# Optimization experiments

Hardware: AMD Instinct MI355X
Metric: run time of the kernel (lower is better)

Reference implementation:

```python
import jax, jax.numpy as jnp
import numpy as np


def setup_inputs() -> dict:
    key = jax.random.key(0)
    k1, k2, k3, k4, k5 = jax.random.split(key, 5)
    N, E, D = 100000, 600000, 128
    h = jax.random.normal(k1, (N, D), dtype=jnp.float32)
    src = jax.random.randint(k2, (E,), 0, N, dtype=jnp.int64)
    dst = jax.random.randint(k3, (E,), 0, N, dtype=jnp.int64)
    W_w = jax.random.normal(k4, (D, D), dtype=jnp.float32) * (1.0 / np.sqrt(D))
    W_b = jax.random.normal(k5, (D,), dtype=jnp.float32) * 0.01
    return {"h": h, "src": src, "dst": dst, "W_w": W_w, "W_b": W_b}


def reference(h, src, dst, W_w, W_b):
    # Project all node features once (N x D GEMM), then gather per edge.
    # score_e = sum_d (W h[src_e] + b)_d * h[dst_e]_d
    Wh = h @ W_w.T + W_b            # [N, D]
    scores = jnp.sum(Wh[src] * h[dst], axis=-1)  # [E]
    return scores
```

## Files before the change

kernel.cpp:

```cpp
#include <hip/hip_runtime.h>
#include <hip/hip_bf16.h>

#define D 128

typedef __attribute__((ext_vector_type(8))) short bf16x8;
typedef __attribute__((ext_vector_type(4))) float f32x4;

__device__ __forceinline__ unsigned int f2bf_bits(float f) {
    union { float f; unsigned int u; } c; c.f = f;
    return (c.u + 0x7fffu + ((c.u >> 16) & 1u)) >> 16;
}
__device__ __forceinline__ unsigned int pack2bf(float a, float b) {
    return f2bf_bits(a) | (f2bf_bits(b) << 16);
}
__device__ __forceinline__ float bf_lo(unsigned int u) {
    union { unsigned int u; float f; } c; c.u = u << 16; return c.f;
}
__device__ __forceinline__ float bf_hi(unsigned int u) {
    union { unsigned int u; float f; } c; c.u = u & 0xffff0000u; return c.f;
}

__global__ __launch_bounds__(256) void wh_mfma_kernel(
    const float* __restrict__ h, const float* __restrict__ W,
    const float* __restrict__ bias, ushort* __restrict__ Wh_bf,
    ushort* __restrict__ h_bf, int N)
{
    __shared__ alignas(16) unsigned char lds_h[64 * 256];
    __shared__ alignas(16) unsigned char lds_w[128 * 256];

    const int t = threadIdx.x;
    const int nodeBase = blockIdx.x * 64;

#pragma unroll
    for (int it = 0; it < 8; ++it) {
        const int idx = t + 256 * it;
        const int row = idx >> 5;
        const int seg = idx & 31;
        const int node = nodeBase + row;
        float4 x = make_float4(0.f, 0.f, 0.f, 0.f);
        if (node < N)
            x = reinterpret_cast<const float4*>(h)[(size_t)node * 32 + seg];
        const uint2 p = make_uint2(pack2bf(x.x, x.y), pack2bf(x.z, x.w));
        const int boff = (seg * 8) ^ ((row & 7) << 4);
        *reinterpret_cast<uint2*>(&lds_h[row * 256 + boff]) = p;
        if (node < N)
            *reinterpret_cast<uint2*>(h_bf + (size_t)node * D + seg * 4) = p;
    }
#pragma unroll
    for (int it = 0; it < 16; ++it) {
        const int idx = t + 256 * it;
        const int row = idx >> 5;
        const int seg = idx & 31;
        const float4 x = reinterpret_cast<const float4*>(W)[idx];
        const uint2 p = make_uint2(pack2bf(x.x, x.y), pack2bf(x.z, x.w));
        const int boff = (seg * 8) ^ ((row & 7) << 4);
        *reinterpret_cast<uint2*>(&lds_w[row * 256 + boff]) = p;
    }
    __syncthreads();

    const int lane = t & 63;
    const int wv   = t >> 6;
    const int lr   = lane & 15;
    const int g    = lane >> 4;

    bf16x8 afrag[4];
    {
        const int row = wv * 16 + lr;
#pragma unroll
        for (int kt = 0; kt < 4; ++kt) {
            const int boff = (kt * 64 + g * 16) ^ ((row & 7) << 4);
            afrag[kt] = *reinterpret_cast<const bf16x8*>(&lds_h[row * 256 + boff]);
        }
    }

#pragma unroll
    for (int ct = 0; ct < 8; ++ct) {
        const int wrow = ct * 16 + lr;
        const float bb = bias[wrow];
        f32x4 acc = {bb, bb, bb, bb};
#pragma unroll
        for (int kt = 0; kt < 4; ++kt) {
            const int boff = (kt * 64 + g * 16) ^ ((wrow & 7) << 4);
            const bf16x8 bfrag =
                *reinterpret_cast<const bf16x8*>(&lds_w[wrow * 256 + boff]);
            acc = __builtin_amdgcn_mfma_f32_16x16x32_bf16(afrag[kt], bfrag, acc, 0, 0, 0);
        }
        const int node0 = nodeBase + wv * 16 + g * 4;
#pragma unroll
        for (int r = 0; r < 4; ++r) {
            if (node0 + r < N)
                Wh_bf[(size_t)(node0 + r) * D + wrow] = (ushort)f2bf_bits(acc[r]);
        }
    }
}

__global__ __launch_bounds__(256) void edge_score_kernel(
    const ushort* __restrict__ Wh_bf, const ushort* __restrict__ h_bf,
    const int* __restrict__ src, const int* __restrict__ dst,
    float* __restrict__ out, int E)
{
    const long long t = (long long)blockIdx.x * blockDim.x + threadIdx.x;
    const int e = (int)(t >> 4);
    const int l = (int)(t & 15);
    if (e >= E) return;

    const int s = src[e];
    const int d = dst[e];

    const uint4 av = reinterpret_cast<const uint4*>(Wh_bf + (size_t)s * D)[l];
    const uint4 bv = reinterpret_cast<const uint4*>(h_bf  + (size_t)d * D)[l];

    float acc = 0.f;
    acc = fmaf(bf_lo(av.x), bf_lo(bv.x), acc);
    acc = fmaf(bf_hi(av.x), bf_hi(bv.x), acc);
    acc = fmaf(bf_lo(av.y), bf_lo(bv.y), acc);
    acc = fmaf(bf_hi(av.y), bf_hi(bv.y), acc);
    acc = fmaf(bf_lo(av.z), bf_lo(bv.z), acc);
    acc = fmaf(bf_hi(av.z), bf_hi(bv.z), acc);
    acc = fmaf(bf_lo(av.w), bf_lo(bv.w), acc);
    acc = fmaf(bf_hi(av.w), bf_hi(bv.w), acc);

#pragma unroll
    for (int m = 8; m > 0; m >>= 1)
        acc += __shfl_xor(acc, m, 64);

    if (l == 0) out[e] = acc;
}

extern "C" void kernel_launch(void* const* d_in, const int* in_sizes, int n_in,
                              void* d_out, int out_size, void* d_ws, size_t ws_size,
                              hipStream_t stream)
{
    const float* h   = (const float*)d_in[0];
    const int*   src = (const int*)  d_in[1];
    const int*   dst = (const int*)  d_in[2];
    const float* W   = (const float*)d_in[3];
    const float* b   = (const float*)d_in[4];
    float* out = (float*)d_out;

    const int N = in_sizes[0] / D;
    const int E = in_sizes[1];

    ushort* Wh_bf = (ushort*)d_ws;
    ushort* h_bf  = (ushort*)d_ws + (size_t)N * D;

    {
        const int blocks = (N + 63) / 64;
        wh_mfma_kernel<<<blocks, 256, 0, stream>>>(h, W, b, Wh_bf, h_bf, N);
    }
    {
        const long long total = (long long)E * 16;
        const int blocks = (int)((total + 255) / 256);
        edge_score_kernel<<<blocks, 256, 0, stream>>>(Wh_bf, h_bf, src, dst, out, E);
    }
}
```

Baseline: 151.0 us.

## Persist GEMM blocks over node tiles and process two edges per 8-lane group

The projection kernel becomes persistent with a grid capped at 768 blocks. Each block converts W into LDS once and loops over 64-node tiles, so the per-block W load and bf16 conversion are amortised. The edge kernel now gives each 8-lane group two edges, with 32 bytes per lane per row, and writes both scores with a single float2 store. That cuts the shuffle reduction and raises memory-level parallelism per thread. bf16 packing switches to the HIP intrinsic conversion. The costs are an extra barrier per tile and less grid-level parallelism in the GEMM.

```diff
diff --git a/kernel.cpp b/kernel.cpp
--- a/kernel.cpp
+++ b/kernel.cpp
@@ -11,7 +11,9 @@
     return (c.u + 0x7fffu + ((c.u >> 16) & 1u)) >> 16;
 }
 __device__ __forceinline__ unsigned int pack2bf(float a, float b) {
-    return f2bf_bits(a) | (f2bf_bits(b) << 16);
+    union { __hip_bfloat162 h; unsigned int u; } c;
+    c.h = __float22bfloat162_rn(make_float2(a, b));
+    return c.u;
 }
 __device__ __forceinline__ float bf_lo(unsigned int u) {
     union { unsigned int u; float f; } c; c.u = u << 16; return c.f;
@@ -20,32 +22,28 @@
     union { unsigned int u; float f; } c; c.u = u & 0xffff0000u; return c.f;
 }
 
+__device__ __forceinline__ float dot8(uint4 a, uint4 b, float acc) {
+    acc = fmaf(bf_lo(a.x), bf_lo(b.x), acc);
+    acc = fmaf(bf_hi(a.x), bf_hi(b.x), acc);
+    acc = fmaf(bf_lo(a.y), bf_lo(b.y), acc);
+    acc = fmaf(bf_hi(a.y), bf_hi(b.y), acc);
+    acc = fmaf(bf_lo(a.z), bf_lo(b.z), acc);
+    acc = fmaf(bf_hi(a.z), bf_hi(b.z), acc);
+    acc = fmaf(bf_lo(a.w), bf_lo(b.w), acc);
+    acc = fmaf(bf_hi(a.w), bf_hi(b.w), acc);
+    return acc;
+}
+
 __global__ __launch_bounds__(256) void wh_mfma_kernel(
     const float* __restrict__ h, const float* __restrict__ W,
     const float* __restrict__ bias, ushort* __restrict__ Wh_bf,
-    ushort* __restrict__ h_bf, int N)
+    ushort* __restrict__ h_bf, int N, int numTiles)
 {
     __shared__ alignas(16) unsigned char lds_h[64 * 256];
     __shared__ alignas(16) unsigned char lds_w[128 * 256];
 
     const int t = threadIdx.x;
-    const int nodeBase = blockIdx.x * 64;
 
-#pragma unroll
-    for (int it = 0; it < 8; ++it) {
-        const int idx = t + 256 * it;
-        const int row = idx >> 5;
-        const int seg = idx & 31;
-        const int node = nodeBase + row;
-        float4 x = make_float4(0.f, 0.f, 0.f, 0.f);
-        if (node < N)
-            x = reinterpret_cast<const float4*>(h)[(size_t)node * 32 + seg];
-        const uint2 p = make_uint2(pack2bf(x.x, x.y), pack2bf(x.z, x.w));
-        const int boff = (seg * 8) ^ ((row & 7) << 4);
-        *reinterpret_cast<uint2*>(&lds_h[row * 256 + boff]) = p;
-        if (node < N)
-            *reinterpret_cast<uint2*>(h_bf + (size_t)node * D + seg * 4) = p;
-    }
 #pragma unroll
     for (int it = 0; it < 16; ++it) {
         const int idx = t + 256 * it;
@@ -56,41 +54,62 @@
         const int boff = (seg * 8) ^ ((row & 7) << 4);
         *reinterpret_cast<uint2*>(&lds_w[row * 256 + boff]) = p;
     }
-    __syncthreads();
 
     const int lane = t & 63;
     const int wv   = t >> 6;
     const int lr   = lane & 15;
     const int g    = lane >> 4;
 
-    bf16x8 afrag[4];
-    {
-        const int row = wv * 16 + lr;
-#pragma unroll
-        for (int kt = 0; kt < 4; ++kt) {
-            const int boff = (kt * 64 + g * 16) ^ ((row & 7) << 4);
-            afrag[kt] = *reinterpret_cast<const bf16x8*>(&lds_h[row * 256 + boff]);
-        }
-    }
+    for (int tile = blockIdx.x; tile < numTiles; tile += gridDim.x) {
+        const int nodeBase = tile * 64;
 
 #pragma unroll
-    for (int ct = 0; ct < 8; ++ct) {
-        const int wrow = ct * 16 + lr;
-        const float bb = bias[wrow];
-        f32x4 acc = {bb, bb, bb, bb};
+        for (int it = 0; it < 8; ++it) {
+            const int idx = t + 256 * it;
+            const int row = idx >> 5;
+            const int seg = idx & 31;
+            const int node = nodeBase + row;
+            float4 x = make_float4(0.f, 0.f, 0.f, 0.f);
+            if (node < N)
+                x = reinterpret_cast<const float4*>(h)[(size_t)node * 32 + seg];
+            const uint2 p = make_uint2(pack2bf(x.x, x.y), pack2bf(x.z, x.w));
+            const int boff = (seg * 8) ^ ((row & 7) << 4);
+            *reinterpret_cast<uint2*>(&lds_h[row * 256 + boff]) = p;
+            if (node < N)
+                *reinterpret_cast<uint2*>(h_bf + (size_t)node * D + seg * 4) = p;
+        }
+        __syncthreads();
+
+        bf16x8 afrag[4];
+        {
+            const int row = wv * 16 + lr;
 #pragma unroll
-        for (int kt = 0; kt < 4; ++kt) {
-            const int boff = (kt * 64 + g * 16) ^ ((wrow & 7) << 4);
-            const bf16x8 bfrag =
-                *reinterpret_cast<const bf16x8*>(&lds_w[wrow * 256 + boff]);
-            acc = __builtin_amdgcn_mfma_f32_16x16x32_bf16(afrag[kt], bfrag, acc, 0, 0, 0);
+            for (int kt = 0; kt < 4; ++kt) {
+                const int boff = (kt * 64 + g * 16) ^ ((row & 7) << 4);
+                afrag[kt] = *reinterpret_cast<const bf16x8*>(&lds_h[row * 256 + boff]);
+            }
         }
-        const int node0 = nodeBase + wv * 16 + g * 4;
+
 #pragma unroll
-        for (int r = 0; r < 4; ++r) {
-            if (node0 + r < N)
-                Wh_bf[(size_t)(node0 + r) * D + wrow] = (ushort)f2bf_bits(acc[r]);
+        for (int ct = 0; ct < 8; ++ct) {
+            const int wrow = ct * 16 + lr;
+            const float bb = bias[wrow];
+            f32x4 acc = {bb, bb, bb, bb};
+#pragma unroll
+            for (int kt = 0; kt < 4; ++kt) {
+                const int boff = (kt * 64 + g * 16) ^ ((wrow & 7) << 4);
+                const bf16x8 bfrag =
+                    *reinterpret_cast<const bf16x8*>(&lds_w[wrow * 256 + boff]);
+                acc = __builtin_amdgcn_mfma_f32_16x16x32_bf16(afrag[kt], bfrag, acc, 0, 0, 0);
+            }
+            const int node0 = nodeBase + wv * 16 + g * 4;
+#pragma unroll
+            for (int r = 0; r < 4; ++r) {
+                if (node0 + r < N)
+                    Wh_bf[(size_t)(node0 + r) * D + wrow] = (ushort)f2bf_bits(acc[r]);
+            }
         }
+        __syncthreads();
     }
 }
 
@@ -100,31 +119,48 @@
     float* __restrict__ out, int E)
 {
     const long long t = (long long)blockIdx.x * blockDim.x + threadIdx.x;
-    const int e = (int)(t >> 4);
-    const int l = (int)(t & 15);
-    if (e >= E) return;
+    const int grp = (int)(t >> 3);
+    const int l   = (int)(t & 7);
+    const int e0  = grp * 2;
+    if (e0 >= E) return;
+    const int e1 = e0 + 1;
+    const bool has1 = e1 < E;
 
-    const int s = src[e];
-    const int d = dst[e];
+    const int s0 = src[e0], d0 = dst[e0];
+    const int s1 = has1 ? src[e1] : s0;
+    const int d1 = has1 ? dst[e1] : d0;
 
-    const uint4 av = reinterpret_cast<const uint4*>(Wh_bf + (size_t)s * D)[l];
-    const uint4 bv = reinterpret_cast<const uint4*>(h_bf  + (size_t)d * D)[l];
+    const uint4* A0 = reinterpret_cast<const uint4*>(Wh_bf + (size_t)s0 * D);
+    const uint4* B0 = reinterpret_cast<const uint4*>(h_bf  + (size_t)d0 * D);
+    const uint4* A1 = reinterpret_cast<const uint4*>(Wh_bf + (size_t)s1 * D);
+    const uint4* B1 = reinterpret_cast<const uint4*>(h_bf  + (size_t)d1 * D);
 
-    float acc = 0.f;
-    acc = fmaf(bf_lo(av.x), bf_lo(bv.x), acc);
-    acc = fmaf(bf_hi(av.x), bf_hi(bv.x), acc);
-    acc = fmaf(bf_lo(av.y), bf_lo(bv.y), acc);
-    acc = fmaf(bf_hi(av.y), bf_hi(bv.y), acc);
-    acc = fmaf(bf_lo(av.z), bf_lo(bv.z), acc);
-    acc = fmaf(bf_hi(av.z), bf_hi(bv.z), acc);
-    acc = fmaf(bf_lo(av.w), bf_lo(bv.w), acc);
-    acc = fmaf(bf_hi(av.w), bf_hi(bv.w), acc);
+    const uint4 a0a = A0[2 * l];
+    const uint4 a0b = A0[2 * l + 1];
+    const uint4 b0a = B0[2 * l];
+    const uint4 b0b = B0[2 * l + 1];
+    const uint4 a1a = A1[2 * l];
+    const uint4 a1b = A1[2 * l + 1];
+    const uint4 b1a = B1[2 * l];
+    const uint4 b1b = B1[2 * l + 1];
+
+    float acc0 = dot8(a0a, b0a, 0.f);
+    acc0 = dot8(a0b, b0b, acc0);
+    float acc1 = dot8(a1a, b1a, 0.f);
+    acc1 = dot8(a1b, b1b, acc1);
 
 #pragma unroll
-    for (int m = 8; m > 0; m >>= 1)
-        acc += __shfl_xor(acc, m, 64);
+    for (int m = 4; m > 0; m >>= 1) {
+        acc0 += __shfl_xor(acc0, m, 64);
+        acc1 += __shfl_xor(acc1, m, 64);
+    }
 
-    if (l == 0) out[e] = acc;
+    if (l == 0) {
+        if (has1)
+            *reinterpret_cast<float2*>(out + e0) = make_float2(acc0, acc1);
+        else
+            out[e0] = acc0;
+    }
 }
 
 extern "C" void kernel_launch(void* const* d_in, const int* in_sizes, int n_in,
@@ -145,11 +181,12 @@
     ushort* h_bf  = (ushort*)d_ws + (size_t)N * D;
 
     {
-        const int blocks = (N + 63) / 64;
-        wh_mfma_kernel<<<blocks, 256, 0, stream>>>(h, W, b, Wh_bf, h_bf, N);
+        const int numTiles = (N + 63) / 64;
+        const int blocks = numTiles < 768 ? numTiles : 768;
+        wh_mfma_kernel<<<blocks, 256, 0, stream>>>(h, W, b, Wh_bf, h_bf, N, numTiles);
     }
     {
-        const long long total = (long long)E * 16;
+        const long long total = ((long long)E + 1) / 2 * 8;
         const int blocks = (int)((total + 255) / 256);
         edge_score_kernel<<<blocks, 256, 0, stream>>>(Wh_bf, h_bf, src, dst, out, E);
     }
```

Result: no change. 148.4 us (-1.7%).
